# Performance work log

Hardware: AMD Instinct MI355X
Metric: run time of the kernel (lower is better)

Reference implementation:

```python
import jax, jax.numpy as jnp
import numpy as np

KROT = 8        # number of pairwise-rotation layers (hard-coded in Rotation)
GROUP = 128     # rotation group size (hard-coded)
QGS = 128       # quantization group size (hard-coded in RotateLinearAWQMarlinInt4)


def setup_inputs() -> dict:
    rng = np.random.default_rng(0)
    M, K, N = 32, 8192, 28672
    G = K // QGS  # 64 quant groups
    shifts = np.arange(8, dtype=np.uint32) * 4
    # activations
    x = jnp.asarray(rng.standard_normal((M, K)), dtype=jnp.float16)
    # int4 weights packed 8-per-int32 along the out dim (nibble j of word n -> column n*8+j)
    nib = rng.integers(0, 16, size=(K, N // 8, 8), dtype=np.uint32)
    qweight = jnp.asarray((nib << shifts).sum(-1, dtype=np.uint32).view(np.int32))  # (K, N//8)
    znib = rng.integers(0, 16, size=(G, N // 8, 8), dtype=np.uint32)
    qzeros = jnp.asarray((znib << shifts).sum(-1, dtype=np.uint32).view(np.int32))  # (G, N//8)
    scales = jnp.asarray(rng.uniform(0.001, 0.01, (G, N)), dtype=jnp.float16)
    bias = jnp.asarray(rng.standard_normal(N) * 0.01, dtype=jnp.float16)
    # rotation params: per-layer angles over all K//2 pairs; one local permutation of
    # 0..127 per layer, shared across all K//GROUP groups (as in Rotation.__init__)
    theta = jnp.asarray(rng.uniform(-0.2, 0.2, (KROT, K // 2)), dtype=jnp.float16)
    pairs = jnp.asarray(np.stack([rng.permutation(GROUP) for _ in range(KROT)]).astype(np.int32))  # (KROT, 128)
    channel_scales = jnp.asarray(rng.uniform(0.5, 2.0, (1, K)), dtype=jnp.float16)
    return dict(x=x, qweight=qweight, qzeros=qzeros, scales=scales, bias=bias,
                theta=theta, pairs=pairs, channel_scales=channel_scales)


def _rotate(x, pairs, theta, channel_scales):
    # x: (M, K). Apply KROT layers of Givens rotations on channel pairs within each
    # 128-wide group, then per-channel scaling.
    M, K = x.shape
    ng = K // GROUP
    xg = x.reshape(M, ng, GROUP)
    for k in range(KROT):
        p = pairs[k]                      # (128,) local permutation
        i, j = p[0::2], p[1::2]           # (64,) disjoint index sets
        th = theta[k].reshape(ng, GROUP // 2).astype(jnp.float32)  # (ng, 64) per-group angles
        c = jnp.cos(th).astype(x.dtype)
        s = jnp.sin(th).astype(x.dtype)
        xi = xg[:, :, i]
        xj = xg[:, :, j]
        xg = xg.at[:, :, i].set(c * xi - s * xj)
        xg = xg.at[:, :, j].set(s * xi + c * xj)
    return xg.reshape(M, K) * channel_scales


def _dequant(qweight, qzeros, scales):
    # unpack 8 uint4 nibbles per int32 along the out dim; dequant per quant group
    K = qweight.shape[0]
    shifts = jnp.arange(8, dtype=jnp.int32) * 4
    w = ((qweight[:, :, None] >> shifts) & 0xF).reshape(K, -1)       # (K, N) ints 0..15
    z = ((qzeros[:, :, None] >> shifts) & 0xF).reshape(qzeros.shape[0], -1)  # (G, N)
    zf = jnp.repeat(z.astype(scales.dtype), QGS, axis=0)             # (K, N)
    sf = jnp.repeat(scales, QGS, axis=0)                             # (K, N)
    return (w.astype(scales.dtype) - zf) * sf


def reference(x, qweight, qzeros, scales, bias, theta, pairs, channel_scales):
    xr = _rotate(x, pairs, theta, channel_scales)   # (M, K)
    W = _dequant(qweight, qzeros, scales)           # (K, N)
    return xr @ W + bias
```

## Files before the change

kernel.cpp:

```cpp
#include <hip/hip_runtime.h>
#include <hip/hip_bf16.h>

using uint32   = unsigned int;
using ushort_t = unsigned short;
using short8   = __attribute__((ext_vector_type(8))) short;
using uint4v   = __attribute__((ext_vector_type(4))) uint32;
using floatx16 = __attribute__((ext_vector_type(16))) float;

#define M_DIM 32
#define K_DIM 8192
#define N_DIM 28672
#define QROW  (N_DIM/8)
#define KSPLIT 8
#define BN    256
#define CH    128
#define NCH   8

typedef __attribute__((address_space(3))) uint32 lds_u32;
typedef const __attribute__((address_space(1))) uint32 glb_u32;

__device__ ushort_t g_xr[M_DIM * K_DIM];
__device__ float    g_S[64 * M_DIM];

__device__ __forceinline__ float bf2f(ushort_t u){
  unsigned int v = ((unsigned int)u) << 16;
  return __builtin_bit_cast(float, v);
}
__device__ __forceinline__ ushort_t f2bf(float f){
  return __builtin_bit_cast(ushort_t, __float2bfloat16(f));
}

__global__ __launch_bounds__(256) void rotate_kernel(
    const float* __restrict__ x, const float* __restrict__ theta,
    const int* __restrict__ pairs, const float* __restrict__ cs)
{
  __shared__ float xb[4][128];
  const int u    = threadIdx.x >> 6;
  const int lane = threadIdx.x & 63;
  const int id   = blockIdx.x * 4 + u;
  const int m    = id >> 6;
  const int g    = id & 63;
  const float* xp = x + m*K_DIM + g*128;
  int   ip[8], jp[8];
  float cv[8], sv[8];
  #pragma unroll
  for (int k = 0; k < 8; ++k){
    ip[k] = pairs[k*128 + 2*lane];
    jp[k] = pairs[k*128 + 2*lane + 1];
    const float th = theta[k*(K_DIM/2) + g*64 + lane];
    cv[k] = cosf(th); sv[k] = sinf(th);
  }
  xb[u][lane]    = xp[lane];
  xb[u][lane+64] = xp[lane+64];
  #pragma unroll
  for (int k = 0; k < 8; ++k){
    __syncthreads();
    const float xi = xb[u][ip[k]], xj = xb[u][jp[k]];
    xb[u][ip[k]] = cv[k]*xi - sv[k]*xj;
    xb[u][jp[k]] = sv[k]*xi + cv[k]*xj;
  }
  __syncthreads();
  const int base = g*128;
  const ushort_t b0 = f2bf(xb[u][lane]    * cs[base+lane]);
  const ushort_t b1 = f2bf(xb[u][lane+64] * cs[base+lane+64]);
  g_xr[m*K_DIM + base + lane]      = b0;
  g_xr[m*K_DIM + base + lane + 64] = b1;
  float sum = bf2f(b0) + bf2f(b1);
  #pragma unroll
  for (int d = 32; d > 0; d >>= 1) sum += __shfl_xor(sum, d, 64);
  if (lane == 0) g_S[g*32 + m] = sum;
}

__global__ __launch_bounds__(256) void init_kernel(
    const float* __restrict__ bias, float* __restrict__ out)
{
  const int n = blockIdx.x*256 + threadIdx.x;
  out[(size_t)blockIdx.y*N_DIM + n] = bias[n];
}

__global__ __launch_bounds__(512) void gemm_kernel(
    const uint32* __restrict__ qw, const uint32* __restrict__ qz,
    const float* __restrict__ scales, float* __restrict__ out)
{
  __shared__ uint32 sq[2][CH*32];
  const int bid  = blockIdx.x;
  const int ks   = bid & 7;
  const int nb   = bid >> 3;
  const int w    = threadIdx.x >> 6;
  const int lane = threadIdx.x & 63;
  const int l31  = lane & 31;
  const int koct = lane >> 5;
  const int n0   = nb * BN;
  const int n    = n0 + w*32 + l31;
  const int col  = n >> 3;
  const uint32 sh = (uint32)((n & 7) * 4);
  const int dwi  = w*4 + (l31 >> 3);
  const int kbase0 = ks * 1024;

  float accT[16];
  #pragma unroll
  for (int r = 0; r < 16; ++r) accT[r] = 0.f;

  auto stage = [&](int c){
    uint32* lp0 = &sq[c & 1][0];
    #pragma unroll
    for (int i = 0; i < 2; ++i){
      const int rl = w*16 + i*8 + (lane >> 3);
      const size_t kglob = (size_t)(kbase0 + c*CH + rl);
      const uint32* gp = qw + kglob*QROW + (n0 >> 3) + (lane & 7)*4;
      uint32* lp = lp0 + (size_t)(w*16 + i*8)*32 + (size_t)lane*4;
      __builtin_amdgcn_global_load_lds((glb_u32*)gp, (lds_u32*)lp, 16, 0, 0);
    }
  };

  stage(0);
  #pragma unroll 1
  for (int c = 0; c < NCH; ++c){
    __syncthreads();
    if (c + 1 < NCH) stage(c + 1);
    const int g = ks*NCH + c;
    const uint32 zq = qz[(size_t)g*QROW + col];
    const float  s  = scales[(size_t)g*N_DIM + n];
    const float  zz = (float)(128u + ((zq >> sh) & 15u));
    const uint32* sqc = &sq[c & 1][0];
    const ushort_t* arow = g_xr + (size_t)l31*K_DIM + kbase0 + c*CH + koct*8;

    floatx16 acc;
    #pragma unroll
    for (int r = 0; r < 16; ++r) acc[r] = 0.f;

    #pragma unroll
    for (int kk8 = 0; kk8 < 8; ++kk8){
      const short8 a = *(const short8*)(arow + kk8*16);
      const int qb = (kk8*16 + koct*8)*32 + dwi;
      const uint32 q0 = sqc[qb], q1 = sqc[qb+32], q2 = sqc[qb+64], q3 = sqc[qb+96];
      const uint32 q4 = sqc[qb+128], q5 = sqc[qb+160], q6 = sqc[qb+192], q7 = sqc[qb+224];
      uint4v bp;
      bp.x = (((q0 >> sh) & 15u) | (((q1 >> sh) & 15u) << 16)) | 0x43004300u;
      bp.y = (((q2 >> sh) & 15u) | (((q3 >> sh) & 15u) << 16)) | 0x43004300u;
      bp.z = (((q4 >> sh) & 15u) | (((q5 >> sh) & 15u) << 16)) | 0x43004300u;
      bp.w = (((q6 >> sh) & 15u) | (((q7 >> sh) & 15u) << 16)) | 0x43004300u;
      const short8 b = __builtin_bit_cast(short8, bp);
      acc = __builtin_amdgcn_mfma_f32_32x32x16_bf16(a, b, acc, 0, 0, 0);
    }
    #pragma unroll
    for (int r = 0; r < 16; ++r){
      const int row = (r & 3) + 8*(r >> 2) + 4*koct;
      const float t = fmaf(-zz, g_S[g*32 + row], acc[r]);
      accT[r] = fmaf(s, t, accT[r]);
    }
  }
  #pragma unroll
  for (int r = 0; r < 16; ++r){
    const int row = (r & 3) + 8*(r >> 2) + 4*koct;
    atomicAdd(out + (size_t)row*N_DIM + n, accT[r]);
  }
}

extern "C" void kernel_launch(void* const* d_in, const int* in_sizes, int n_in,
                              void* d_out, int out_size, void* d_ws, size_t ws_size,
                              hipStream_t stream)
{
  const float*  x      = (const float*)d_in[0];
  const uint32* qw     = (const uint32*)d_in[1];
  const uint32* qz     = (const uint32*)d_in[2];
  const float*  scales = (const float*)d_in[3];
  const float*  bias   = (const float*)d_in[4];
  const float*  theta  = (const float*)d_in[5];
  const int*    pairs  = (const int*)d_in[6];
  const float*  cs     = (const float*)d_in[7];
  float* out = (float*)d_out;

  rotate_kernel<<<dim3((M_DIM*64)/4), dim3(256), 0, stream>>>(x, theta, pairs, cs);
  init_kernel<<<dim3(N_DIM/256, M_DIM), dim3(256), 0, stream>>>(bias, out);
  gemm_kernel<<<dim3((N_DIM/BN)*KSPLIT), dim3(512), 0, stream>>>(qw, qz, scales, out);
}
```

Before: 252.2 us.

## Transpose weights in LDS, tile activations, and move zero-point correction to init

The rotate kernel now writes activations in a k-octet-major tiled layout, so the GEMM can stage them into LDS with direct global-to-LDS loads. Weight words are loaded into registers and transposed into a padded LDS tile, so each lane reads its eight k-values with two vector LDS loads instead of eight scalar ones. The zero-point times row-sum correction and the bias are computed once per column in a new init kernel, which removes the qzeros loads and per-group g_S work from the GEMM inner loop. In exchange the GEMM gains an extra barrier per chunk and register-staged prefetching, and the init kernel does 64 groups × 32 rows of FMAs per column over only 112 blocks.

```diff
diff --git a/kernel.cpp b/kernel.cpp
--- a/kernel.cpp
+++ b/kernel.cpp
@@ -15,11 +15,12 @@
 #define BN    256
 #define CH    128
 #define NCH   8
+#define TSTRIDE 132
 
 typedef __attribute__((address_space(3))) uint32 lds_u32;
 typedef const __attribute__((address_space(1))) uint32 glb_u32;
 
-__device__ ushort_t g_xr[M_DIM * K_DIM];
+__device__ ushort_t g_xr2[M_DIM * K_DIM];
 __device__ float    g_S[64 * M_DIM];
 
 __device__ __forceinline__ float bf2f(ushort_t u){
@@ -61,93 +62,123 @@
   }
   __syncthreads();
   const int base = g*128;
-  const ushort_t b0 = f2bf(xb[u][lane]    * cs[base+lane]);
-  const ushort_t b1 = f2bf(xb[u][lane+64] * cs[base+lane+64]);
-  g_xr[m*K_DIM + base + lane]      = b0;
-  g_xr[m*K_DIM + base + lane + 64] = b1;
+  const int k0 = base + lane, k1 = base + lane + 64;
+  const ushort_t b0 = f2bf(xb[u][lane]    * cs[k0]);
+  const ushort_t b1 = f2bf(xb[u][lane+64] * cs[k1]);
+  g_xr2[(((size_t)(k0>>3))*32 + m)*8 + (k0&7)] = b0;
+  g_xr2[(((size_t)(k1>>3))*32 + m)*8 + (k1&7)] = b1;
   float sum = bf2f(b0) + bf2f(b1);
   #pragma unroll
   for (int d = 32; d > 0; d >>= 1) sum += __shfl_xor(sum, d, 64);
-  if (lane == 0) g_S[g*32 + m] = sum;
-}
-
-__global__ __launch_bounds__(256) void init_kernel(
+  if (lane == 0) g_S[g*M_DIM + m] = sum;
+}
+
+__global__ __launch_bounds__(256) void init2_kernel(
+    const uint32* __restrict__ qz, const float* __restrict__ scales,
     const float* __restrict__ bias, float* __restrict__ out)
 {
   const int n = blockIdx.x*256 + threadIdx.x;
-  out[(size_t)blockIdx.y*N_DIM + n] = bias[n];
-}
-
-__global__ __launch_bounds__(512) void gemm_kernel(
-    const uint32* __restrict__ qw, const uint32* __restrict__ qz,
-    const float* __restrict__ scales, float* __restrict__ out)
-{
-  __shared__ uint32 sq[2][CH*32];
+  const uint32 sh = (uint32)((n & 7)*4);
+  float acc[M_DIM];
+  const float b = bias[n];
+  #pragma unroll
+  for (int m = 0; m < M_DIM; ++m) acc[m] = b;
+  #pragma unroll 1
+  for (int g = 0; g < 64; ++g){
+    const float s  = scales[(size_t)g*N_DIM + n];
+    const uint32 zq = qz[(size_t)g*QROW + (n>>3)];
+    const float t  = s * (float)(128u + ((zq >> sh) & 15u));
+    #pragma unroll
+    for (int m = 0; m < M_DIM; ++m)
+      acc[m] = fmaf(-t, g_S[g*M_DIM + m], acc[m]);
+  }
+  #pragma unroll
+  for (int m = 0; m < M_DIM; ++m) out[(size_t)m*N_DIM + n] = acc[m];
+}
+
+__global__ __launch_bounds__(512, 4) void gemm_kernel(
+    const uint32* __restrict__ qw, const float* __restrict__ scales,
+    float* __restrict__ out)
+{
+  __shared__ uint32   T[32*TSTRIDE];
+  __shared__ ushort_t A[2][CH*32];
   const int bid  = blockIdx.x;
   const int ks   = bid & 7;
   const int nb   = bid >> 3;
-  const int w    = threadIdx.x >> 6;
-  const int lane = threadIdx.x & 63;
+  const int tid  = threadIdx.x;
+  const int w    = tid >> 6;
+  const int lane = tid & 63;
   const int l31  = lane & 31;
   const int koct = lane >> 5;
   const int n0   = nb * BN;
   const int n    = n0 + w*32 + l31;
-  const int col  = n >> 3;
-  const uint32 sh = (uint32)((n & 7) * 4);
-  const int dwi  = w*4 + (l31 >> 3);
-  const int kbase0 = ks * 1024;
+  const uint32 sh = (uint32)((l31 & 7)*4);
+  const int col  = w*4 + (l31 >> 3);
+  const int k0   = ks * (NCH*CH);
+
+  const int brow = tid >> 3;
+  const int bcq  = tid & 7;
+  const uint32* bbase = qw + (size_t)(k0 + brow)*QROW + (n0>>3) + bcq*4;
+  const ushort_t* abase = g_xr2 + (size_t)k0*32;
 
   float accT[16];
   #pragma unroll
   for (int r = 0; r < 16; ++r) accT[r] = 0.f;
 
-  auto stage = [&](int c){
-    uint32* lp0 = &sq[c & 1][0];
-    #pragma unroll
-    for (int i = 0; i < 2; ++i){
-      const int rl = w*16 + i*8 + (lane >> 3);
-      const size_t kglob = (size_t)(kbase0 + c*CH + rl);
-      const uint32* gp = qw + kglob*QROW + (n0 >> 3) + (lane & 7)*4;
-      uint32* lp = lp0 + (size_t)(w*16 + i*8)*32 + (size_t)lane*4;
-      __builtin_amdgcn_global_load_lds((glb_u32*)gp, (lds_u32*)lp, 16, 0, 0);
-    }
+  uint4v bv[2][2];
+
+  auto stageA = [&](int c){
+    const ushort_t* gp = abase + (size_t)c*CH*32 + w*512 + lane*8;
+    ushort_t* lp = &A[c & 1][0] + w*512;
+    __builtin_amdgcn_global_load_lds((glb_u32*)gp, (lds_u32*)lp, 16, 0, 0);
   };
 
-  stage(0);
-  #pragma unroll 1
+  bv[0][0] = *(const uint4v*)(bbase);
+  bv[0][1] = *(const uint4v*)(bbase + (size_t)64*QROW);
+  stageA(0);
+  #pragma unroll
+  for (int j = 0; j < 4; ++j){
+    T[(bcq*4 + j)*TSTRIDE + brow]      = bv[0][0][j];
+    T[(bcq*4 + j)*TSTRIDE + brow + 64] = bv[0][1][j];
+  }
+
+  #pragma unroll
   for (int c = 0; c < NCH; ++c){
     __syncthreads();
-    if (c + 1 < NCH) stage(c + 1);
-    const int g = ks*NCH + c;
-    const uint32 zq = qz[(size_t)g*QROW + col];
-    const float  s  = scales[(size_t)g*N_DIM + n];
-    const float  zz = (float)(128u + ((zq >> sh) & 15u));
-    const uint32* sqc = &sq[c & 1][0];
-    const ushort_t* arow = g_xr + (size_t)l31*K_DIM + kbase0 + c*CH + koct*8;
-
+    const int cb = c & 1, nx = cb ^ 1;
+    if (c + 1 < NCH){
+      const uint32* bb = bbase + (size_t)(c+1)*CH*QROW;
+      bv[nx][0] = *(const uint4v*)(bb);
+      bv[nx][1] = *(const uint4v*)(bb + (size_t)64*QROW);
+      stageA(c+1);
+    }
+    const float s = scales[(size_t)(ks*NCH + c)*N_DIM + n];
     floatx16 acc;
     #pragma unroll
     for (int r = 0; r < 16; ++r) acc[r] = 0.f;
-
-    #pragma unroll
-    for (int kk8 = 0; kk8 < 8; ++kk8){
-      const short8 a = *(const short8*)(arow + kk8*16);
-      const int qb = (kk8*16 + koct*8)*32 + dwi;
-      const uint32 q0 = sqc[qb], q1 = sqc[qb+32], q2 = sqc[qb+64], q3 = sqc[qb+96];
-      const uint32 q4 = sqc[qb+128], q5 = sqc[qb+160], q6 = sqc[qb+192], q7 = sqc[qb+224];
+    #pragma unroll
+    for (int kk = 0; kk < 8; ++kk){
+      const short8 a = *(const short8*)(&A[cb][((kk*2 + koct)*32 + l31)*8]);
+      const uint32* tp = &T[col*TSTRIDE + kk*16 + koct*8];
+      const uint4v p0 = *(const uint4v*)(tp);
+      const uint4v p1 = *(const uint4v*)(tp + 4);
       uint4v bp;
-      bp.x = (((q0 >> sh) & 15u) | (((q1 >> sh) & 15u) << 16)) | 0x43004300u;
-      bp.y = (((q2 >> sh) & 15u) | (((q3 >> sh) & 15u) << 16)) | 0x43004300u;
-      bp.z = (((q4 >> sh) & 15u) | (((q5 >> sh) & 15u) << 16)) | 0x43004300u;
-      bp.w = (((q6 >> sh) & 15u) | (((q7 >> sh) & 15u) << 16)) | 0x43004300u;
-      const short8 b = __builtin_bit_cast(short8, bp);
-      acc = __builtin_amdgcn_mfma_f32_32x32x16_bf16(a, b, acc, 0, 0, 0);
+      bp.x = ((p0.x >> sh) & 15u) | (((p0.y >> sh) & 15u) << 16) | 0x43004300u;
+      bp.y = ((p0.z >> sh) & 15u) | (((p0.w >> sh) & 15u) << 16) | 0x43004300u;
+      bp.z = ((p1.x >> sh) & 15u) | (((p1.y >> sh) & 15u) << 16) | 0x43004300u;
+      bp.w = ((p1.z >> sh) & 15u) | (((p1.w >> sh) & 15u) << 16) | 0x43004300u;
+      acc = __builtin_amdgcn_mfma_f32_32x32x16_bf16(
+                a, __builtin_bit_cast(short8, bp), acc, 0, 0, 0);
     }
     #pragma unroll
-    for (int r = 0; r < 16; ++r){
-      const int row = (r & 3) + 8*(r >> 2) + 4*koct;
-      const float t = fmaf(-zz, g_S[g*32 + row], acc[r]);
-      accT[r] = fmaf(s, t, accT[r]);
+    for (int r = 0; r < 16; ++r) accT[r] = fmaf(s, acc[r], accT[r]);
+    __syncthreads();
+    if (c + 1 < NCH){
+      #pragma unroll
+      for (int j = 0; j < 4; ++j){
+        T[(bcq*4 + j)*TSTRIDE + brow]      = bv[nx][0][j];
+        T[(bcq*4 + j)*TSTRIDE + brow + 64] = bv[nx][1][j];
+      }
     }
   }
   #pragma unroll
@@ -172,6 +203,6 @@
   float* out = (float*)d_out;
 
   rotate_kernel<<<dim3((M_DIM*64)/4), dim3(256), 0, stream>>>(x, theta, pairs, cs);
-  init_kernel<<<dim3(N_DIM/256, M_DIM), dim3(256), 0, stream>>>(bias, out);
-  gemm_kernel<<<dim3((N_DIM/BN)*KSPLIT), dim3(512), 0, stream>>>(qw, qz, scales, out);
-}
+  init2_kernel<<<dim3(N_DIM/256), dim3(256), 0, stream>>>(qz, scales, bias, out);
+  gemm_kernel<<<dim3((N_DIM/BN)*KSPLIT), dim3(512), 0, stream>>>(qw, scales, out);
+}
```

Measured after the change: 247.7 us. No clear change (-1.8%).
